# Kernel optimization log

Measured on AMD Instinct MI355X. Metric: run time of the kernel, lower is better.

## Reference

```python
import jax, jax.numpy as jnp
import numpy as np

MODE1 = 12
MODE2 = 12
WIDTH = 64
L = 10
DEPTH = 4
PAD = 9
EPS = 1e-5


def conv1x1(x, w, b):
    # x: (B,Ci,H,W), w: (Co,Ci), b: (Co,)
    return jnp.einsum('oi,bihw->bohw', w, x) + b[None, :, None, None]


def group_norm(x, gamma, beta, groups=2):
    B, C, H, W = x.shape
    xg = x.reshape(B, groups, C // groups, H, W)
    mu = xg.mean(axis=(2, 3, 4), keepdims=True)
    var = xg.var(axis=(2, 3, 4), keepdims=True)
    xn = ((xg - mu) * jax.lax.rsqrt(var + EPS)).reshape(B, C, H, W)
    return xn * gamma[None, :, None, None] + beta[None, :, None, None]


def spectral_conv(x, w1, w2):
    # x: (B,Ci,H,W); w1,w2: (Ci,Co,m1,m2,2) real/imag stacked
    B, Ci, H, W = x.shape
    Co = w1.shape[1]
    x_ft = jnp.fft.rfft2(x)  # (B,Ci,H,W//2+1) complex
    w1c = w1[..., 0] + 1j * w1[..., 1]
    w2c = w2[..., 0] + 1j * w2[..., 1]
    t1 = jnp.einsum('bixy,ioxy->boxy', x_ft[:, :, :MODE1, :MODE2], w1c)
    t2 = jnp.einsum('bixy,ioxy->boxy', x_ft[:, :, -MODE1:, :MODE2], w2c)
    out_ft = jnp.zeros((B, Co, H, W // 2 + 1), dtype=x_ft.dtype)
    out_ft = out_ft.at[:, :, :MODE1, :MODE2].set(t1)
    out_ft = out_ft.at[:, :, -MODE1:, :MODE2].set(t2)
    return jnp.fft.irfft2(out_ft, s=(H, W))


def mlp_block(x, w1, b1, g, bt, w2, b2):
    x = conv1x1(x, w1, b1)
    x = group_norm(x, g, bt)
    x = jax.nn.gelu(x, approximate=False)
    return conv1x1(x, w2, b2)


def get_grid(B, S):
    gx = jnp.linspace(0.0, 1.0, S, dtype=jnp.float32)
    gy = jnp.linspace(0.0, 1.0, S, dtype=jnp.float32)
    gridx = jnp.broadcast_to(gx[None, :, None, None], (B, S, S, 1))
    gridy = jnp.broadcast_to(gy[None, None, :, None], (B, S, S, 1))
    return jnp.concatenate([gridx, gridy], axis=-1)  # (B,S,S,2)


def pos_encoding(grid):
    # grid: (B,S,S,2) -> (B,S,S,4L); cos over all L then sin over all L,
    # within each L the 2 grid channels stay adjacent (matches torch cat order)
    freqs = (jnp.pi * (2.0 ** jnp.arange(L))).astype(jnp.float32)  # (L,)
    phase = grid[..., None, :] * freqs[:, None]  # (B,S,S,L,2)
    B, S1, S2 = grid.shape[:3]
    phase = phase.reshape(B, S1, S2, L * 2)
    return jnp.concatenate([jnp.cos(phase), jnp.sin(phase)], axis=-1)


def setup_inputs() -> dict:
    key = jax.random.key(0)
    ks = jax.random.split(key, 24)
    B, S = 8, 192
    Cin = 3 + 4 * L  # 43
    Wd = WIDTH
    scale = 1.0 / (Wd * Wd)
    d = {}
    d['x'] = jax.random.normal(ks[0], (B, S, S, 1), dtype=jnp.float32)
    d['Wp'] = jax.random.normal(ks[1], (Cin, Wd), dtype=jnp.float32) / np.sqrt(Cin)
    d['bp'] = jnp.zeros((Wd,), dtype=jnp.float32)
    d['sw1'] = scale * jax.random.uniform(ks[2], (DEPTH, Wd, Wd, MODE1, MODE2, 2), dtype=jnp.float32)
    d['sw2'] = scale * jax.random.uniform(ks[3], (DEPTH, Wd, Wd, MODE1, MODE2, 2), dtype=jnp.float32)
    d['m1w'] = jax.random.normal(ks[4], (DEPTH, Wd, Wd), dtype=jnp.float32) / np.sqrt(Wd)
    d['m1b'] = jnp.zeros((DEPTH, Wd), dtype=jnp.float32)
    d['mg'] = jnp.ones((DEPTH, Wd), dtype=jnp.float32)
    d['mbt'] = jnp.zeros((DEPTH, Wd), dtype=jnp.float32)
    d['m2w'] = jax.random.normal(ks[5], (DEPTH, Wd, Wd), dtype=jnp.float32) / np.sqrt(Wd)
    d['m2b'] = jnp.zeros((DEPTH, Wd), dtype=jnp.float32)
    d['ww'] = jax.random.normal(ks[6], (DEPTH, Wd, Wd), dtype=jnp.float32) / np.sqrt(Wd)
    d['wb'] = jnp.zeros((DEPTH, Wd), dtype=jnp.float32)
    d['ng'] = jnp.ones((DEPTH, Wd), dtype=jnp.float32)
    d['nb'] = jnp.zeros((DEPTH, Wd), dtype=jnp.float32)
    Wq = Wd * 4
    d['q1w'] = jax.random.normal(ks[7], (Wq, Wd), dtype=jnp.float32) / np.sqrt(Wd)
    d['q1b'] = jnp.zeros((Wq,), dtype=jnp.float32)
    d['qg'] = jnp.ones((Wq,), dtype=jnp.float32)
    d['qbt'] = jnp.zeros((Wq,), dtype=jnp.float32)
    d['q2w'] = jax.random.normal(ks[8], (1, Wq), dtype=jnp.float32) / np.sqrt(Wq)
    d['q2b'] = jnp.zeros((1,), dtype=jnp.float32)
    return d


def reference(x, Wp, bp, sw1, sw2, m1w, m1b, mg, mbt, m2w, m2b, ww, wb, ng, nb,
              q1w, q1b, qg, qbt, q2w, q2b):
    B, S = x.shape[0], x.shape[1]
    grid = get_grid(B, S)
    pe = pos_encoding(grid)
    h = jnp.concatenate([x, grid, pe], axis=-1)  # (B,S,S,43)
    h = h @ Wp + bp  # lift
    h = h.transpose(0, 3, 1, 2)  # (B,W,S,S)
    h = jnp.pad(h, ((0, 0), (0, 0), (0, PAD), (0, PAD)))
    for i in range(DEPTH):
        x1 = spectral_conv(h, sw1[i], sw2[i])
        x1 = mlp_block(x1, m1w[i], m1b[i], mg[i], mbt[i], m2w[i], m2b[i])
        x2 = conv1x1(h, ww[i], wb[i])
        x2 = group_norm(x2, ng[i], nb[i])
        h = x1 + x2
        if i != DEPTH - 1:
            h = jax.nn.gelu(h, approximate=False)
    h = h[..., :-PAD, :-PAD]
    h = mlp_block(h, q1w, q1b, qg, qbt, q2w, q2b)
    return h.transpose(0, 2, 3, 1)  # (B,S,S,1)
```

## Files before the change

kernel.cpp:

```cpp
#include <hip/hip_runtime.h>
#include <hip/hip_bf16.h>
#include <math.h>


#define NN 201
#define SS 192
#define NPIX 40401
#define QPIX 36864
#define BB 8
#define GNB 80
#define XWPL 1234944
#define PI_F 3.14159265358979323846f

typedef __hip_bfloat16 bf16;
typedef __attribute__((ext_vector_type(8))) short s8v;
typedef __attribute__((ext_vector_type(4))) float f32x4;

__device__ __forceinline__ float gelu_f(float x){
  float x2 = x*x;
  float t  = fmaf(x2, 0.0713548162f, 1.5957691216f);
  float e  = __expf(-x*t);
  return x*__builtin_amdgcn_rcpf(1.0f+e);
}
__device__ __forceinline__ float b2f(bf16 v){ return __bfloat162float(v); }
__device__ __forceinline__ bf16  f2b(float v){ return __float2bfloat16(v); }
__device__ __forceinline__ unsigned short f2bu(float x){
  bf16 h = __float2bfloat16(x);
  unsigned short u; __builtin_memcpy(&u,&h,2); return u;
}
__device__ __forceinline__ float bu2f(unsigned short u){
  unsigned int x = ((unsigned int)u)<<16; float f; __builtin_memcpy(&f,&x,4); return f;
}

__global__ void k_tab(float* __restrict__ tab){
  int t = blockIdx.x*blockDim.x+threadIdx.x;
  if(t>=13*NN) return;
  int k=t/NN, n=t-k*NN;
  int m=(k*n)%NN;
  float ang = (2.0f*PI_F/201.0f)*(float)m;
  tab[2*t]   = cosf(ang);
  tab[2*t+1] = sinf(ang);
}

__global__ void k_tpack(const float* __restrict__ tab, unsigned short* __restrict__ TPK){
  int e = blockIdx.x*256 + threadIdx.x;
  if(e>=6656) return;
  int wt=e>>9, lane=(e>>3)&63, j=e&7;
  int m_=lane&15, g=lane>>4;
  int w = wt*16+m_;
  int k24 = g*8+j;
  float v=0.f;
  if(k24<24 && w<201){
    float2 cs = ((const float2*)tab)[(k24>>1)*NN + w];
    v = (k24&1)? cs.y : cs.x;
  }
  TPK[e]=f2bu(v);
}

__global__ void k_pretab(const float* __restrict__ Wp, const float* __restrict__ bp,
                         float* __restrict__ Ux, float* __restrict__ Uy){
  int i = blockIdx.x;
  int ax = blockIdx.y;
  int c = threadIdx.x;
  float g = (float)i*(1.0f/191.0f);
  float acc;
  if(ax==0) acc = bp[c] + g*Wp[64+c];
  else      acc = g*Wp[128+c];
  int cosBase = (ax==0)? 3 : 4;
  int sinBase = (ax==0)? 23 : 24;
  #pragma unroll
  for(int l=0;l<10;l++){
    float f = PI_F*(float)(1<<l);
    float sv,cv;
    sincosf(g*f,&sv,&cv);
    acc += cv*Wp[(cosBase+2*l)*64+c] + sv*Wp[(sinBase+2*l)*64+c];
  }
  float* U = (ax==0)? Ux : Uy;
  U[i*64+c] = acc;
}

__global__ void k_wpack(const float* __restrict__ m1w, const float* __restrict__ m2w,
                        const float* __restrict__ ww,  const float* __restrict__ q1w,
                        unsigned short* __restrict__ WPK){
  int bx = blockIdx.x, tid = threadIdx.x;
  const float* src;
  if(bx<12){
    int l=bx/3, sel=bx-l*3;
    src = (sel==0)? m1w+(size_t)l*4096 : (sel==1)? m2w+(size_t)l*4096 : ww+(size_t)l*4096;
  } else {
    src = q1w + (size_t)(bx-12)*4096;
  }
  unsigned short* dst = WPK + (size_t)bx*4096;
  #pragma unroll
  for(int t=0;t<16;t++){
    int d = tid*16+t;
    int frag=d>>9, lane=(d>>3)&63, j=d&7;
    int mt=frag>>1, kh=frag&1, m_=lane&15, g=lane>>4;
    dst[d] = f2bu(src[(size_t)(16*mt+m_)*64 + 32*kh + 8*g + j]);
  }
}

__global__ void __launch_bounds__(256) k_wtrans(const float* __restrict__ w1,
        const float* __restrict__ w2, float* __restrict__ WT){
  __shared__ float tile[64][65];
  int io0 = blockIdx.x*64;
  int c0  = blockIdx.y*64;
  int z   = blockIdx.z;
  const float* src = (z==0)? w1 : w2;
  int tid = threadIdx.x;
  #pragma unroll
  for(int it=0;it<16;it++){
    int e = tid + 256*it;
    int r = e>>6, c = e&63;
    if(c0+c<288) tile[r][c] = src[(size_t)(io0+r)*288 + c0 + c];
  }
  __syncthreads();
  #pragma unroll
  for(int it=0;it<16;it++){
    int e = tid + 256*it;
    int rp = e>>6, cp = e&63;
    int col = c0 + rp;
    if(col<288){
      int ky = col/24, rm = col - ky*24;
      int kx = rm>>1, comp = rm&1;
      int m = z*144 + ky*12 + kx;
      WT[(size_t)m*8192 + comp*4096 + io0 + cp] = tile[cp][rp];
    }
  }
}

__global__ void k_encoder(const float* __restrict__ x, const float* __restrict__ Wp,
                          const float* __restrict__ Ux, const float* __restrict__ Uy,
                          bf16* __restrict__ A){
  int tid=threadIdx.x;
  int p = blockIdx.x*256+tid;
  if(p>=NPIX) return;
  int b = blockIdx.y;
  uint4* dst = (uint4*)(A + ((size_t)b*NPIX + p)*64);
  int hh=p/NN, ww=p-hh*NN;
  if(hh>=SS || ww>=SS){
    uint4 z = {0,0,0,0};
    #pragma unroll
    for(int i=0;i<8;i++) dst[i]=z;
    return;
  }
  float xv = x[((size_t)b*SS+hh)*SS+ww];
  const float4* ux = (const float4*)(Ux + hh*64);
  const float4* uy = (const float4*)(Uy + ww*64);
  const float4* w0 = (const float4*)Wp;
  #pragma unroll
  for(int i=0;i<8;i++){
    float4 a0 = ux[2*i],   a1 = ux[2*i+1];
    float4 b0 = uy[2*i],   b1 = uy[2*i+1];
    float4 c0 = w0[2*i],   c1 = w0[2*i+1];
    float v0=xv*c0.x+a0.x+b0.x, v1=xv*c0.y+a0.y+b0.y;
    float v2=xv*c0.z+a0.z+b0.z, v3=xv*c0.w+a0.w+b0.w;
    float v4=xv*c1.x+a1.x+b1.x, v5=xv*c1.y+a1.y+b1.y;
    float v6=xv*c1.z+a1.z+b1.z, v7=xv*c1.w+a1.w+b1.w;
    uint4 v;
    v.x = (unsigned)f2bu(v0) | ((unsigned)f2bu(v1)<<16);
    v.y = (unsigned)f2bu(v2) | ((unsigned)f2bu(v3)<<16);
    v.z = (unsigned)f2bu(v4) | ((unsigned)f2bu(v5)<<16);
    v.w = (unsigned)f2bu(v6) | ((unsigned)f2bu(v7)<<16);
    dst[i]=v;
  }
}

__global__ void __launch_bounds__(256) k_dftw(const bf16* __restrict__ A,
        const float* __restrict__ tab, float* __restrict__ XW){
  __shared__ float2 st[2412];
  int tid=threadIdx.x;
  for(int i=tid;i<2412;i+=256) st[i]=((const float2*)tab)[i];
  __syncthreads();
  int R = blockIdx.x*4 + (tid>>6);
  int l = tid&63;
  const bf16* base = A + ((size_t)R*NN)*64 + l;
  float ar0=0.f;
  float ar[11], ai[11];
  #pragma unroll
  for(int k=0;k<11;k++){ ar[k]=0.f; ai[k]=0.f; }
  for(int w=0;w<NN;w++){
    float a = b2f(base[(size_t)w*64]);
    ar0 += a;
    #pragma unroll
    for(int k=0;k<11;k++){
      float2 cs = st[(k+1)*NN+w];
      ar[k] += a*cs.x;
      ai[k] += a*cs.y;
    }
  }
  float* xre = XW + ((size_t)R*12)*64 + l;
  float* xim = xre + XWPL;
  xre[0]=ar0; xim[0]=0.f;
  #pragma unroll
  for(int k=0;k<11;k++){
    xre[(size_t)(k+1)*64] = ar[k];
    xim[(size_t)(k+1)*64] = -ai[k];
  }
}

__global__ void __launch_bounds__(256) k_dfth(const float* __restrict__ XW,
        const float* __restrict__ tab, float* __restrict__ XF){
  __shared__ float sre[201*32];
  __shared__ float sim[201*32];
  __shared__ float2 tw[13*NN];
  int kx=blockIdx.x, b=blockIdx.y;
  int z=blockIdx.z; int jh=z>>1, ch=z&1;
  int tid=threadIdx.x;
  for(int i=tid;i<13*NN;i+=256) tw[i]=((const float2*)tab)[i];
  for(int i=tid;i<201*32;i+=256){
    int h=i>>5, c=ch*32+(i&31);
    size_t idx=(((size_t)b*NN+h)*12+kx)*64+c;
    sre[i]=XW[idx];
    sim[i]=XW[idx+XWPL];
  }
  __syncthreads();
  for(int o=tid;o<384;o+=256){
    int jj=o>>5, cl=o&31;
    int j=jh*12+jj;
    int k2=(j<12)?j:24-j;
    float sgn=(j<12)?-1.f:1.f;
    float re0=0.f,im0=0.f,re1=0.f,im1=0.f;
    const float* pr=sre+cl;
    const float* pi=sim+cl;
    const float2* tk=tw+k2*NN;
    int h=0;
    for(;h+1<NN;h+=2){
      float a0=pr[h*32], b0=pi[h*32];
      float2 cs0=tk[h];
      float c0=cs0.x, s0=sgn*cs0.y;
      re0 = fmaf(a0,c0, fmaf(-b0,s0, re0));
      im0 = fmaf(a0,s0, fmaf( b0,c0, im0));
      float a1=pr[(h+1)*32], b1=pi[(h+1)*32];
      float2 cs1=tk[h+1];
      float c1=cs1.x, s1=sgn*cs1.y;
      re1 = fmaf(a1,c1, fmaf(-b1,s1, re1));
      im1 = fmaf(a1,s1, fmaf( b1,c1, im1));
    }
    {
      float a0=pr[h*32], b0=pi[h*32];
      float2 cs0=tk[h];
      float c0=cs0.x, s0=sgn*cs0.y;
      re0 = fmaf(a0,c0, fmaf(-b0,s0, re0));
      im0 = fmaf(a0,s0, fmaf( b0,c0, im0));
    }
    int m=j*12+kx;
    int c=ch*32+cl;
    XF[(size_t)m*1024+(b*64+c)*2]  =re0+re1;
    XF[(size_t)m*1024+(b*64+c)*2+1]=im0+im1;
  }
}

__global__ void __launch_bounds__(512) k_modemix(const float* __restrict__ XF,
     const float* __restrict__ WT, float* __restrict__ XO){
  __shared__ float sx[1024];
  __shared__ float swr[4096], swi[4096];
  int m=blockIdx.x;
  int tid=threadIdx.x;
  sx[tid]     = XF[(size_t)m*1024+tid];
  sx[tid+512] = XF[(size_t)m*1024+tid+512];
  const float* wr = WT + (size_t)m*8192;
  const float* wi = wr + 4096;
  for(int io=tid;io<4096;io+=512){
    swr[io]=wr[io];
    swi[io]=wi[io];
  }
  __syncthreads();
  int b=tid>>6, o=tid&63;
  const float* xb = sx + b*128;
  float re0=0.f,re1=0.f,im0=0.f,im1=0.f;
  #pragma unroll 8
  for(int i=0;i<64;i+=2){
    float a=xb[2*i], b2=xb[2*i+1];
    float c=swr[i*64+o], d=swi[i*64+o];
    re0 = fmaf(a,c, fmaf(-b2,d, re0));
    im0 = fmaf(a,d, fmaf( b2,c, im0));
    float a1=xb[2*i+2], b3=xb[2*i+3];
    float c1=swr[(i+1)*64+o], d1=swi[(i+1)*64+o];
    re1 = fmaf(a1,c1, fmaf(-b3,d1, re1));
    im1 = fmaf(a1,d1, fmaf( b3,c1, im1));
  }
  XO[2*((size_t)m*512+tid)]  =re0+re1;
  XO[2*((size_t)m*512+tid)+1]=im0+im1;
}

__global__ void __launch_bounds__(256) k_ispec(const float* __restrict__ XO,
        const float* __restrict__ tab, const unsigned short* __restrict__ TPK,
        bf16* __restrict__ C){
  __shared__ float2 yl[12][64];
  __shared__ float2 cs13[13];
  int R=blockIdx.x;
  int b=R/NN, h=R-b*NN;
  int tid=threadIdx.x;
  if(tid<13) cs13[tid]=((const float2*)tab)[tid*NN+h];
  __syncthreads();
  const float sc = 1.0f/40401.0f;
  #pragma unroll
  for(int it=0;it<3;it++){
    int item = tid + 256*it;
    int kx = item>>6, o = item&63;
    float re0=0.f,im0=0.f,re1=0.f,im1=0.f;
    #pragma unroll
    for(int j=0;j<24;j+=2){
      {
        int k2=(j<12)?j:24-j;
        float sgn=(j<12)?1.0f:-1.0f;
        float2 xo = *(const float2*)(XO + 2*(((size_t)(j*12+kx)*512) + b*64 + o));
        float2 cs = cs13[k2];
        float cc=cs.x, s2=sgn*cs.y;
        re0 = fmaf(xo.x,cc, fmaf(-xo.y,s2, re0));
        im0 = fmaf(xo.x,s2, fmaf( xo.y,cc, im0));
      }
      {
        int j1=j+1;
        int k2=(j1<12)?j1:24-j1;
        float sgn=(j1<12)?1.0f:-1.0f;
        float2 xo = *(const float2*)(XO + 2*(((size_t)(j1*12+kx)*512) + b*64 + o));
        float2 cs = cs13[k2];
        float cc=cs.x, s2=sgn*cs.y;
        re1 = fmaf(xo.x,cc, fmaf(-xo.y,s2, re1));
        im1 = fmaf(xo.x,s2, fmaf( xo.y,cc, im1));
      }
    }
    float fr = (kx==0)? sc : 2.0f*sc;
    float fi = (kx==0)? sc : -2.0f*sc;
    yl[kx][o] = float2{ (re0+re1)*fr, (im0+im1)*fi };
  }
  __syncthreads();
  int wid=tid>>6, l=tid&63, m_=l&15, g=l>>4;
  int o = wid*16 + m_;
  s8v bfr;
  #pragma unroll
  for(int j=0;j<4;j++){
    float2 v = yl[4*g+j][o];
    bfr[2*j]   = (short)f2bu(v.x);
    bfr[2*j+1] = (short)f2bu(v.y);
  }
  bf16* cp = C + (size_t)R*NN*64;
  #pragma unroll
  for(int wt=0; wt<13; wt++){
    s8v af = *(const s8v*)(TPK + (size_t)wt*512 + l*8);
    f32x4 acc = f32x4{0.f,0.f,0.f,0.f};
    acc = __builtin_amdgcn_mfma_f32_16x16x32_bf16(af, bfr, acc, 0,0,0);
    #pragma unroll
    for(int e=0;e<4;e++){
      int w = wt*16 + 4*g + e;
      if(w<NN) cp[(size_t)w*64 + o] = f2b(acc[e]);
    }
  }
}

__global__ void __launch_bounds__(256) k_gramC(const float* __restrict__ XO,
        float* __restrict__ GCp, float* __restrict__ SC){
  __shared__ unsigned short V[64][72];
  int chunk=blockIdx.x, b=blockIdx.y, tid=threadIdx.x;
  const float s1=1.0f/201.0f;
  const float r2=0.70710678118f;
  const float q2=1.41421356237f;
  #pragma unroll
  for(int it=0;it<16;it++){
    int e = tid + it*256;
    int fl=e>>6, ch=e&63;
    int f = chunk*64 + fl;
    int base = b*64+ch;
    float v=0.f;
    if(f<528){
      int comp=f&1, kxm=f>>1;
      int kx0=kxm/24;
      int kx=1+kx0, m=kxm-kx0*24;
      v = q2*XO[2*((size_t)(m*12+kx)*512 + base)+comp];
    } else if(f==528){
      v = XO[2*(size_t)base];
    } else if(f<551){
      int q=f-529; int mm=1+(q>>1);
      const float* p1 = XO + 2*((size_t)(mm*12)*512 + base);
      const float* p2 = XO + 2*((size_t)((24-mm)*12)*512 + base);
      v = ((q&1)==0)? r2*(p1[0]+p2[0]) : r2*(p1[1]-p2[1]);
    } else if(f==551){
      v = r2*XO[2*((size_t)(144)*512 + base)];
    } else if(f==552){
      v = r2*XO[2*((size_t)(144)*512 + base)+1];
    }
    V[ch][fl]=f2bu(v*s1);
  }
  __syncthreads();
  int wid=tid>>6, l=tid&63, m_=l&15, g=l>>4;
  f32x4 acc[4];
  #pragma unroll
  for(int mt=0;mt<4;mt++) acc[mt]=f32x4{0.f,0.f,0.f,0.f};
  #pragma unroll
  for(int kc=0;kc<2;kc++){
    s8v bfr = *(const s8v*)&V[16*wid+m_][kc*32+8*g];
    #pragma unroll
    for(int mt=0;mt<4;mt++){
      s8v afr = *(const s8v*)&V[16*mt+m_][kc*32+8*g];
      acc[mt]=__builtin_amdgcn_mfma_f32_16x16x32_bf16(afr,bfr,acc[mt],0,0,0);
    }
  }
  float* gb = GCp + ((size_t)(b*9+chunk))*4096;
  #pragma unroll
  for(int mt=0;mt<4;mt++){
    #pragma unroll
    for(int e=0;e<4;e++)
      gb[(size_t)(16*mt+4*g+e)*64 + 16*wid + m_] = acc[mt][e];
  }
  if(chunk==0 && tid<64) SC[b*64+tid] = XO[2*(size_t)(b*64+tid)];
}

__global__ void k_gcred(const float* __restrict__ GCp, float* __restrict__ GC){
  int b=blockIdx.y;
  int idx=blockIdx.x*256+threadIdx.x;
  float s=0.f;
  #pragma unroll
  for(int k=0;k<9;k++) s += GCp[((size_t)(b*9+k))*4096 + idx];
  GC[(size_t)b*4096 + idx]=s;
}

__global__ void __launch_bounds__(256) k_gramp(const bf16* __restrict__ X,
        float* __restrict__ Gpart, float* __restrict__ Spart, int HR, int WR){
  int b = blockIdx.y, blk = blockIdx.x;
  int npix = HR*WR;
  int tid=threadIdx.x, wid=tid>>6, l=tid&63;
  int m_=l&15, g=l>>4;
  int slab = blk*4 + wid;
  const bf16* xb = X + (size_t)b*NPIX*64;
  f32x4 acc[4][4];
  #pragma unroll
  for(int mt=0;mt<4;mt++){
    #pragma unroll
    for(int nt=0;nt<4;nt++) acc[mt][nt]=f32x4{0.f,0.f,0.f,0.f};
  }
  float cs[4]={0.f,0.f,0.f,0.f};
  for(int kc=0;kc<16;kc++){
    int pbase = slab*512 + kc*32 + g*8;
    int hh0=0, ww0=0;
    if(WR!=NN){ hh0 = pbase/WR; ww0 = pbase - hh0*WR; }
    const bf16* ptr[8];
    #pragma unroll
    for(int jj=0;jj<8;jj++){
      int p = pbase + jj;
      int gp;
      if(WR==NN) gp = p;
      else {
        int ww2 = ww0 + jj;
        int hh  = hh0;
        if(ww2>=WR){ ww2-=WR; hh++; }
        gp = hh*NN + ww2;
      }
      ptr[jj] = (p<npix) ? (xb + (size_t)gp*64) : (const bf16*)0;
    }
    s8v fr[4];
    #pragma unroll
    for(int t=0;t<4;t++){
      s8v f;
      float s=0.f;
      #pragma unroll
      for(int jj=0;jj<8;jj++){
        unsigned short v=0;
        if(ptr[jj]){ bf16 hv = ptr[jj][16*t+m_]; __builtin_memcpy(&v,&hv,2); }
        f[jj]=(short)v;
        s += bu2f(v);
      }
      fr[t]=f;
      cs[t]+=s;
    }
    #pragma unroll
    for(int nt=0;nt<4;nt++){
      #pragma unroll
      for(int mt=0;mt<4;mt++)
        acc[mt][nt]=__builtin_amdgcn_mfma_f32_16x16x32_bf16(fr[mt],fr[nt],acc[mt][nt],0,0,0);
    }
  }
  float* gp_ = Gpart + ((size_t)(b*GNB + slab))*4096;
  #pragma unroll
  for(int mt=0;mt<4;mt++){
    #pragma unroll
    for(int nt=0;nt<4;nt++){
      #pragma unroll
      for(int e=0;e<4;e++)
        gp_[(size_t)(16*mt + 4*g + e)*64 + 16*nt + m_] = acc[mt][nt][e];
    }
  }
  #pragma unroll
  for(int t=0;t<4;t++){
    float s=cs[t];
    s += __shfl_xor(s,16,64);
    s += __shfl_xor(s,32,64);
    if(g==0) Spart[((size_t)(b*GNB+slab))*64 + 16*t + m_] = s;
  }
}

__global__ void __launch_bounds__(256) k_gramr(const float* __restrict__ Gpart,
        const float* __restrict__ Spart, float* __restrict__ Gfin,
        float* __restrict__ Sfin, int nblk){
  int b = blockIdx.y;
  int idx = blockIdx.x*256 + threadIdx.x;
  float s0=0.f,s1=0.f,s2=0.f,s3=0.f;
  int k=0;
  for(;k+3<nblk;k+=4){
    s0 += Gpart[((size_t)b*GNB + k  )*4096 + idx];
    s1 += Gpart[((size_t)b*GNB + k+1)*4096 + idx];
    s2 += Gpart[((size_t)b*GNB + k+2)*4096 + idx];
    s3 += Gpart[((size_t)b*GNB + k+3)*4096 + idx];
  }
  for(;k<nblk;k++) s0 += Gpart[((size_t)b*GNB + k)*4096 + idx];
  Gfin[(size_t)b*4096 + idx] = (s0+s1)+(s2+s3);
  if(blockIdx.x==0 && threadIdx.x<64){
    float ss=0.f;
    for(int j=0;j<nblk;j++) ss += Spart[((size_t)b*GNB + j)*64 + threadIdx.x];
    Sfin[b*64 + threadIdx.x]=ss;
  }
}

__global__ void __launch_bounds__(256) k_statsA(
        const float* __restrict__ GC, const float* __restrict__ SC,
        const float* __restrict__ Gfin, const float* __restrict__ Sfin,
        const float* __restrict__ m1wl, const float* __restrict__ m1bl,
        const float* __restrict__ wwl,  const float* __restrict__ wbl,
        float* __restrict__ TSTAT, float* __restrict__ USTAT){
  __shared__ float Gs[4096];
  __shared__ float Ss[64];
  __shared__ float rs[256], rq[256];
  int zb=blockIdx.x, t=threadIdx.x;
  const float* GS = (zb<8)? (GC + (size_t)zb*4096) : (Gfin + (size_t)(zb-8)*4096);
  const float* SS_ = (zb<8)? (SC + (size_t)zb*64)   : (Sfin + (size_t)(zb-8)*64);
  #pragma unroll
  for(int e=0;e<16;e++) Gs[t*16+e]=GS[t*16+e];
  if(t<64) Ss[t]=SS_[t];
  __syncthreads();
  const float* W    = (zb<8)? m1wl : wwl;
  const float* bias = (zb<8)? m1bl : wbl;
  float* stat       = (zb<8)? TSTAT : USTAT;
  int b = (zb<8)? zb : zb-8;
  int o = t&63, sl = t>>6;
  float w[64];
  #pragma unroll
  for(int j2=0;j2<64;j2++) w[j2]=bu2f(f2bu(W[(size_t)o*64+j2]));
  const float* Gr = Gs + (size_t)(sl*16)*64;
  float quad=0.f;
  #pragma unroll
  for(int r=0;r<16;r++){
    const float* gr = Gr + r*64;
    float tt=0.f;
    #pragma unroll
    for(int j2=0;j2<64;j2++) tt += gr[j2]*w[j2];
    quad += w[sl*16+r]*tt;
  }
  float dot=0.f;
  #pragma unroll
  for(int j2=0;j2<64;j2++) dot += w[j2]*Ss[j2];
  float bo = bias[o];
  float Nf = (float)NPIX;
  float sm = (sl==0)? (dot + Nf*bo) : 0.f;
  float sq = quad + ((sl==0)? (2.f*bo*dot + Nf*bo*bo) : 0.f);
  rs[t]=sm; rq[t]=sq;
  __syncthreads();
  if(t<64){
    float s2 = rs[t]+rs[t+64]+rs[t+128]+rs[t+192];
    float q2 = rq[t]+rq[t+64]+rq[t+128]+rq[t+192];
    for(int off=16;off>0;off>>=1){
      s2 += __shfl_down(s2,off,32);
      q2 += __shfl_down(q2,off,32);
    }
    if((t&31)==0){
      int g=t>>5;
      float invN = 1.f/(Nf*32.f);
      float mean = s2*invN;
      float var = q2*invN - mean*mean;
      stat[b*4+g*2]   = mean;
      stat[b*4+g*2+1] = rsqrtf(fmaxf(var,0.f)+1e-5f);
    }
  }
}

__global__ void __launch_bounds__(256) k_statsQ(const float* __restrict__ Gfin,
        const float* __restrict__ Sfin,
        const float* __restrict__ W, const float* __restrict__ bias,
        float* __restrict__ stat){
  __shared__ float Gs[4096];
  __shared__ float Ss[64];
  __shared__ float red[8];
  int b=blockIdx.x, t=threadIdx.x;
  #pragma unroll
  for(int e=0;e<16;e++) Gs[t*16+e]=Gfin[(size_t)b*4096 + t*16+e];
  if(t<64) Ss[t]=Sfin[b*64+t];
  __syncthreads();
  float w[64];
  #pragma unroll
  for(int j2=0;j2<64;j2++) w[j2]=bu2f(f2bu(W[(size_t)t*64+j2]));
  float quad=0.f;
  #pragma unroll
  for(int i=0;i<64;i++){
    const float* gr = Gs + i*64;
    float tt=0.f;
    #pragma unroll
    for(int j2=0;j2<64;j2++) tt += gr[j2]*w[j2];
    quad += w[i]*tt;
  }
  float dot=0.f;
  #pragma unroll
  for(int j2=0;j2<64;j2++) dot += w[j2]*Ss[j2];
  float bo=bias[t];
  float Nf=(float)QPIX;
  float sm = dot + Nf*bo;
  float sq = quad + 2.f*bo*dot + Nf*bo*bo;
  for(int off=32;off>0;off>>=1){
    sm += __shfl_down(sm,off,64);
    sq += __shfl_down(sq,off,64);
  }
  int wid=t>>6;
  if((t&63)==0){ red[wid*2]=sm; red[wid*2+1]=sq; }
  __syncthreads();
  if(t<2){
    float smt = red[t*4+0]+red[t*4+2];
    float sqt = red[t*4+1]+red[t*4+3];
    float invN = 1.f/(Nf*128.f);
    float mean = smt*invN;
    float var = sqt*invN - mean*mean;
    stat[b*4+t*2]   = mean;
    stat[b*4+t*2+1] = rsqrtf(fmaxf(var,0.f)+1e-5f);
  }
}

__global__ void __launch_bounds__(256) k_fuse(const bf16* __restrict__ Cb,
    bf16* __restrict__ A,
    const unsigned short* __restrict__ wp1, const float* __restrict__ m1b,
    const float* __restrict__ mg,  const float* __restrict__ mbt,
    const unsigned short* __restrict__ wp2, const float* __restrict__ m2b,
    const unsigned short* __restrict__ wpw, const float* __restrict__ wbk,
    const float* __restrict__ ng,  const float* __restrict__ nb,
    const float* __restrict__ tstat, const float* __restrict__ ustat, int last){
  __shared__ unsigned short vlds[4][64][72];
  int tid=threadIdx.x;
  int wid=tid>>6, l=tid&63;
  int m_=l&15, g=l>>4;
  int b=blockIdx.y;
  int p0=blockIdx.x*256 + wid*64;
  const bf16* cbb = Cb + (size_t)b*NPIX*64;
  const bf16* ab  = A  + (size_t)b*NPIX*64;

  s8v af[4][2];
  f32x4 acc[4][4];

  #pragma unroll
  for(int mt=0;mt<4;mt++){
    #pragma unroll
    for(int kh=0;kh<2;kh++)
      af[mt][kh]=*(const s8v*)(wp1 + (mt*2+kh)*512 + l*8);
    float4 b4 = *(const float4*)(m1b + 16*mt + 4*g);
    #pragma unroll
    for(int nt=0;nt<4;nt++) acc[mt][nt]=f32x4{b4.x,b4.y,b4.z,b4.w};
  }
  #pragma unroll
  for(int nt=0;nt<4;nt++){
    int p = p0 + 16*nt + m_;
    int pc = p<NPIX? p : NPIX-1;
    const s8v* xb = (const s8v*)(cbb + (size_t)pc*64);
    s8v b0 = xb[g], b1 = xb[4+g];
    #pragma unroll
    for(int mt=0;mt<4;mt++){
      acc[mt][nt]=__builtin_amdgcn_mfma_f32_16x16x32_bf16(af[mt][0],b0,acc[mt][nt],0,0,0);
      acc[mt][nt]=__builtin_amdgcn_mfma_f32_16x16x32_bf16(af[mt][1],b1,acc[mt][nt],0,0,0);
    }
  }
  {
    float tm0=tstat[b*4],tr0=tstat[b*4+1],tm1=tstat[b*4+2],tr1=tstat[b*4+3];
    #pragma unroll
    for(int mt=0;mt<4;mt++){
      float4 g4 = *(const float4*)(mg  + 16*mt + 4*g);
      float4 t4 = *(const float4*)(mbt + 16*mt + 4*g);
      float mn = (mt<2)? tm0 : tm1;
      float rs = (mt<2)? tr0 : tr1;
      float ax=rs*g4.x, ay=rs*g4.y, az=rs*g4.z, aw=rs*g4.w;
      float cx=t4.x-mn*ax, cy=t4.y-mn*ay, cz=t4.z-mn*az, cw=t4.w-mn*aw;
      #pragma unroll
      for(int nt=0;nt<4;nt++){
        int pl = 16*nt + m_;
        f32x4 t = acc[mt][nt];
        float v0 = gelu_f(fmaf(t[0],ax,cx));
        float v1 = gelu_f(fmaf(t[1],ay,cy));
        float v2 = gelu_f(fmaf(t[2],az,cz));
        float v3 = gelu_f(fmaf(t[3],aw,cw));
        uint2 pk;
        pk.x = (unsigned)f2bu(v0) | ((unsigned)f2bu(v1)<<16);
        pk.y = (unsigned)f2bu(v2) | ((unsigned)f2bu(v3)<<16);
        *(uint2*)&vlds[wid][pl][16*mt+4*g] = pk;
      }
    }
  }
  __syncthreads();
  #pragma unroll
  for(int mt=0;mt<4;mt++){
    #pragma unroll
    for(int kh=0;kh<2;kh++)
      af[mt][kh]=*(const s8v*)(wpw + (mt*2+kh)*512 + l*8);
    float4 b4 = *(const float4*)(wbk + 16*mt + 4*g);
    #pragma unroll
    for(int nt=0;nt<4;nt++) acc[mt][nt]=f32x4{b4.x,b4.y,b4.z,b4.w};
  }
  #pragma unroll
  for(int nt=0;nt<4;nt++){
    int p = p0 + 16*nt + m_;
    int pc = p<NPIX? p : NPIX-1;
    const s8v* xb = (const s8v*)(ab + (size_t)pc*64);
    s8v b0 = xb[g], b1 = xb[4+g];
    #pragma unroll
    for(int mt=0;mt<4;mt++){
      acc[mt][nt]=__builtin_amdgcn_mfma_f32_16x16x32_bf16(af[mt][0],b0,acc[mt][nt],0,0,0);
      acc[mt][nt]=__builtin_amdgcn_mfma_f32_16x16x32_bf16(af[mt][1],b1,acc[mt][nt],0,0,0);
    }
  }
  {
    float um0=ustat[b*4],ur0=ustat[b*4+1],um1=ustat[b*4+2],ur1=ustat[b*4+3];
    #pragma unroll
    for(int mt=0;mt<4;mt++){
      float4 n4 = *(const float4*)(ng  + 16*mt + 4*g);
      float4 nb4= *(const float4*)(nb  + 16*mt + 4*g);
      float4 m24= *(const float4*)(m2b + 16*mt + 4*g);
      float mn = (mt<2)? um0 : um1;
      float rs = (mt<2)? ur0 : ur1;
      float ax=rs*n4.x, ay=rs*n4.y, az=rs*n4.z, aw=rs*n4.w;
      float cx=m24.x+nb4.x-mn*ax, cy=m24.y+nb4.y-mn*ay;
      float cz=m24.z+nb4.z-mn*az, cw=m24.w+nb4.w-mn*aw;
      #pragma unroll
      for(int nt=0;nt<4;nt++){
        f32x4 u = acc[mt][nt];
        u[0] = fmaf(u[0],ax,cx);
        u[1] = fmaf(u[1],ay,cy);
        u[2] = fmaf(u[2],az,cz);
        u[3] = fmaf(u[3],aw,cw);
        acc[mt][nt]=u;
      }
    }
  }
  #pragma unroll
  for(int mt=0;mt<4;mt++){
    #pragma unroll
    for(int kh=0;kh<2;kh++)
      af[mt][kh]=*(const s8v*)(wp2 + (mt*2+kh)*512 + l*8);
  }
  #pragma unroll
  for(int nt=0;nt<4;nt++){
    int pl = 16*nt + m_;
    const s8v* vp = (const s8v*)&vlds[wid][pl][0];
    s8v b0 = vp[g], b1 = vp[4+g];
    #pragma unroll
    for(int mt=0;mt<4;mt++){
      acc[mt][nt]=__builtin_amdgcn_mfma_f32_16x16x32_bf16(af[mt][0],b0,acc[mt][nt],0,0,0);
      acc[mt][nt]=__builtin_amdgcn_mfma_f32_16x16x32_bf16(af[mt][1],b1,acc[mt][nt],0,0,0);
    }
  }
  #pragma unroll
  for(int nt=0;nt<4;nt++){
    int p = p0 + 16*nt + m_;
    if(p>=NPIX) continue;
    bf16* dp = A + ((size_t)b*NPIX + p)*64;
    #pragma unroll
    for(int mt=0;mt<4;mt++){
      f32x4 h = acc[mt][nt];
      float h0=h[0],h1=h[1],h2=h[2],h3=h[3];
      if(!last){ h0=gelu_f(h0); h1=gelu_f(h1); h2=gelu_f(h2); h3=gelu_f(h3); }
      uint2 pk;
      pk.x = (unsigned)f2bu(h0) | ((unsigned)f2bu(h1)<<16);
      pk.y = (unsigned)f2bu(h2) | ((unsigned)f2bu(h3)<<16);
      *(uint2*)(dp + 16*mt + 4*g) = pk;
    }
  }
}

__global__ void __launch_bounds__(256) k_qout(const bf16* __restrict__ A,
    const unsigned short* __restrict__ qpack, const float* __restrict__ q1b,
    const float* __restrict__ qg, const float* __restrict__ qbt,
    const float* __restrict__ q2w, const float* __restrict__ q2b,
    const float* __restrict__ qstat, float* __restrict__ out){
  __shared__ unsigned short xq[128][72];
  __shared__ float part[4][128];
  int tid=threadIdx.x;
  int wid=tid>>6, l=tid&63;
  int m_=l&15, g=l>>4;
  int b=blockIdx.y;
  int px0=blockIdx.x*128;
  {
    int p = px0 + (tid>>1);
    int half = tid&1;
    int hh=p/SS, ww2=p-hh*SS;
    const uint4* src=(const uint4*)(A + (((size_t)b*NPIX) + (size_t)hh*NN + ww2)*64 + half*32);
    uint4* drow=(uint4*)&xq[tid>>1][half*32];
    #pragma unroll
    for(int i=0;i<4;i++) drow[i]=src[i];
  }
  __syncthreads();
  int oc=wid;
  const unsigned short* wp = qpack + (size_t)oc*4096;
  s8v af[4][2];
  f32x4 bi4[4];
  float4 a4[4], c4[4], w4[4];
  float m0=qstat[b*4],r0=qstat[b*4+1],m1=qstat[b*4+2],r1=qstat[b*4+3];
  float mn=(oc<2)?m0:m1, rs=(oc<2)?r0:r1;
  #pragma unroll
  for(int mt=0;mt<4;mt++){
    #pragma unroll
    for(int kh=0;kh<2;kh++)
      af[mt][kh]=*(const s8v*)(wp + (mt*2+kh)*512 + l*8);
    float4 b4=*(const float4*)(q1b + 64*oc + 16*mt + 4*g);
    bi4[mt]=f32x4{b4.x,b4.y,b4.z,b4.w};
    float4 g4=*(const float4*)(qg  + 64*oc + 16*mt + 4*g);
    float4 t4=*(const float4*)(qbt + 64*oc + 16*mt + 4*g);
    w4[mt]=*(const float4*)(q2w + 64*oc + 16*mt + 4*g);
    a4[mt]=float4{rs*g4.x, rs*g4.y, rs*g4.z, rs*g4.w};
    c4[mt]=float4{t4.x-mn*a4[mt].x, t4.y-mn*a4[mt].y, t4.z-mn*a4[mt].z, t4.w-mn*a4[mt].w};
  }
  #pragma unroll
  for(int nt=0;nt<8;nt++){
    const s8v* vp = (const s8v*)&xq[16*nt+m_][0];
    s8v b0=vp[g], b1=vp[4+g];
    f32x4 acc[4];
    #pragma unroll
    for(int mt=0;mt<4;mt++) acc[mt]=bi4[mt];
    #pragma unroll
    for(int mt=0;mt<4;mt++){
      acc[mt]=__builtin_amdgcn_mfma_f32_16x16x32_bf16(af[mt][0],b0,acc[mt],0,0,0);
      acc[mt]=__builtin_amdgcn_mfma_f32_16x16x32_bf16(af[mt][1],b1,acc[mt],0,0,0);
    }
    float pp=0.f;
    #pragma unroll
    for(int mt=0;mt<4;mt++){
      f32x4 t=acc[mt];
      pp += gelu_f(fmaf(t[0],a4[mt].x,c4[mt].x))*w4[mt].x;
      pp += gelu_f(fmaf(t[1],a4[mt].y,c4[mt].y))*w4[mt].y;
      pp += gelu_f(fmaf(t[2],a4[mt].z,c4[mt].z))*w4[mt].z;
      pp += gelu_f(fmaf(t[3],a4[mt].w,c4[mt].w))*w4[mt].w;
    }
    pp += __shfl_xor(pp,16,64);
    pp += __shfl_xor(pp,32,64);
    if(g==0) part[wid][16*nt+m_]=pp;
  }
  __syncthreads();
  if(tid<128)
    out[(size_t)b*QPIX + px0 + tid] =
        q2b[0] + part[0][tid]+part[1][tid]+part[2][tid]+part[3][tid];
}

extern "C" void kernel_launch(void* const* d_in, const int* in_sizes, int n_in,
                              void* d_out, int out_size, void* d_ws, size_t ws_size,
                              hipStream_t stream){
  const float* x   = (const float*)d_in[0];
  const float* Wp  = (const float*)d_in[1];
  const float* bp  = (const float*)d_in[2];
  const float* sw1 = (const float*)d_in[3];
  const float* sw2 = (const float*)d_in[4];
  const float* m1w = (const float*)d_in[5];
  const float* m1b = (const float*)d_in[6];
  const float* mg  = (const float*)d_in[7];
  const float* mbt = (const float*)d_in[8];
  const float* m2w = (const float*)d_in[9];
  const float* m2b = (const float*)d_in[10];
  const float* ww  = (const float*)d_in[11];
  const float* wb  = (const float*)d_in[12];
  const float* ng  = (const float*)d_in[13];
  const float* nb  = (const float*)d_in[14];
  const float* q1w = (const float*)d_in[15];
  const float* q1b = (const float*)d_in[16];
  const float* qg  = (const float*)d_in[17];
  const float* qbt = (const float*)d_in[18];
  const float* q2w = (const float*)d_in[19];
  const float* q2b = (const float*)d_in[20];
  float* out = (float*)d_out;

  char* w8 = (char*)d_ws;
  const size_t ACT_B = (size_t)64*BB*NPIX*sizeof(bf16);
  bf16*  A    = (bf16*)(w8);
  bf16*  Cb   = (bf16*)(w8 + ACT_B);
  float* SPEC = (float*)(w8 + 2*ACT_B);
  float* XF   = (float*)(w8 + 2*ACT_B + 9879552);
  float* XO   = (float*)(w8 + 2*ACT_B + 9879552 + 1179648);
  float* TB   = (float*)(w8 + 2*ACT_B + 9879552 + 2*1179648);
  char*  g8   = w8 + 2*ACT_B + 9879552 + 2*1179648 + 20992;
  float* TSTAT= (float*)g8;
  float* USTAT= TSTAT + 32;
  float* QSTAT= USTAT + 32;
  float* UxT  = QSTAT + 32;
  float* UyT  = UxT + 12288;
  unsigned short* WPK = (unsigned short*)(UyT + 12288);
  float* GC   = (float*)(WPK + 16*4096);
  float* SC   = GC + 8*4096;
  float* GFIN = SC + 8*64;
  float* SFIN = GFIN + 8*4096;
  unsigned short* TPK = (unsigned short*)(SFIN + 8*64);
  float* GCp  = SPEC;
  float* Gpart = SPEC;
  float* Spart = Gpart + (size_t)8*GNB*4096;
  float* WT = SPEC;
  size_t needed = (size_t)(2*ACT_B) + 9879552 + 2*1179648 + 20992
                + 3*32*4 + 2*12288*4 + 16*4096*2 + 2*(8*4096+8*64)*4 + 13312;
  if(ws_size < needed) return;

  k_tab<<<11,256,0,stream>>>(TB);
  k_tpack<<<26,256,0,stream>>>(TB, TPK);
  k_pretab<<<dim3(192,2),64,0,stream>>>(Wp, bp, UxT, UyT);
  k_wpack<<<16,256,0,stream>>>(m1w, m2w, ww, q1w, WPK);
  k_encoder<<<dim3(158,BB),256,0,stream>>>(x, Wp, UxT, UyT, A);

  for(int l=0;l<4;l++){
    const float* sw1l = sw1 + (size_t)l*1179648;
    const float* sw2l = sw2 + (size_t)l*1179648;
    k_dftw<<<402,256,0,stream>>>(A, TB, SPEC);
    k_dfth<<<dim3(12,BB,4),256,0,stream>>>(SPEC, TB, XF);
    k_wtrans<<<dim3(64,5,2),256,0,stream>>>(sw1l, sw2l, WT);
    k_modemix<<<288,512,0,stream>>>(XF, WT, XO);
    k_ispec<<<1608,256,0,stream>>>(XO, TB, TPK, Cb);
    k_gramC<<<dim3(9,BB),256,0,stream>>>(XO, GCp, SC);
    k_gcred<<<dim3(16,BB),256,0,stream>>>(GCp, GC);
    k_gramp<<<dim3(20,BB),256,0,stream>>>(A, Gpart, Spart, NN, NN);
    k_gramr<<<dim3(16,BB),256,0,stream>>>(Gpart, Spart, GFIN, SFIN, 80);
    k_statsA<<<16,256,0,stream>>>(GC, SC, GFIN, SFIN,
          m1w + (size_t)l*4096, m1b + l*64, ww + (size_t)l*4096, wb + l*64,
          TSTAT, USTAT);
    k_fuse<<<dim3(158,BB),256,0,stream>>>(Cb, A,
          WPK + (size_t)(l*3+0)*4096, m1b + l*64, mg + l*64, mbt + l*64,
          WPK + (size_t)(l*3+1)*4096, m2b + l*64,
          WPK + (size_t)(l*3+2)*4096, wb  + l*64, ng + l*64, nb + l*64,
          TSTAT, USTAT, (l==3)?1:0);
  }

  k_gramp<<<dim3(18,BB),256,0,stream>>>(A, Gpart, Spart, SS, SS);
  k_gramr<<<dim3(16,BB),256,0,stream>>>(Gpart, Spart, GFIN, SFIN, 72);
  k_statsQ<<<BB,256,0,stream>>>(GFIN, SFIN, q1w, q1b, QSTAT);
  k_qout<<<dim3(288,BB),256,0,stream>>>(A, WPK + (size_t)12*4096, q1b,
          qg, qbt, q2w, q2b, QSTAT, out);
}
```

Measured before the change: 981.5 us.

## Compute width-direction truncated DFT with bf16 MFMA instead of scalar FMA

Replaces the scalar per-lane DFT along the width axis in k_dftw with 16x16x32 bf16 MFMA instructions. A new setup kernel prepacks the cos/-sin twiddle table into MFMA A-fragment layout, and the activations are gathered into B fragments in 32-wide chunks with zero padding on the tail. The goal is to cut the FMA-heavy inner loop and its LDS twiddle reads. In exchange the twiddles are rounded to bf16, which loses accuracy, and the strided per-element fragment gathers may limit the benefit.

Result: faster. 885.8 us (-9.7%).

```diff
diff --git a/kernel.cpp b/kernel.cpp
--- a/kernel.cpp
+++ b/kernel.cpp
@@ -55,6 +55,23 @@
     v = (k24&1)? cs.y : cs.x;
   }
   TPK[e]=f2bu(v);
+}
+
+__global__ void k_tpack2(const float* __restrict__ tab, unsigned short* __restrict__ T2PK){
+  int e = blockIdx.x*256 + threadIdx.x;
+  if(e>=7168) return;
+  int idx = e>>9;
+  int mt = idx/7, chunk = idx - mt*7;
+  int lane=(e>>3)&63, j=e&7;
+  int m_=lane&15, g=lane>>4;
+  int kx24 = mt*16 + m_;
+  int w = chunk*32 + g*8 + j;
+  float v=0.f;
+  if(kx24<24 && w<NN){
+    float2 cs = ((const float2*)tab)[(kx24>>1)*NN + w];
+    v = (kx24&1)? -cs.y : cs.x;
+  }
+  T2PK[e]=f2bu(v);
 }
 
 __global__ void k_pretab(const float* __restrict__ Wp, const float* __restrict__ bp,
@@ -167,35 +184,70 @@
 }
 
 __global__ void __launch_bounds__(256) k_dftw(const bf16* __restrict__ A,
-        const float* __restrict__ tab, float* __restrict__ XW){
-  __shared__ float2 st[2412];
-  int tid=threadIdx.x;
-  for(int i=tid;i<2412;i+=256) st[i]=((const float2*)tab)[i];
-  __syncthreads();
-  int R = blockIdx.x*4 + (tid>>6);
-  int l = tid&63;
-  const bf16* base = A + ((size_t)R*NN)*64 + l;
-  float ar0=0.f;
-  float ar[11], ai[11];
-  #pragma unroll
-  for(int k=0;k<11;k++){ ar[k]=0.f; ai[k]=0.f; }
-  for(int w=0;w<NN;w++){
-    float a = b2f(base[(size_t)w*64]);
-    ar0 += a;
-    #pragma unroll
-    for(int k=0;k<11;k++){
-      float2 cs = st[(k+1)*NN+w];
-      ar[k] += a*cs.x;
-      ai[k] += a*cs.y;
-    }
-  }
-  float* xre = XW + ((size_t)R*12)*64 + l;
-  float* xim = xre + XWPL;
-  xre[0]=ar0; xim[0]=0.f;
-  #pragma unroll
-  for(int k=0;k<11;k++){
-    xre[(size_t)(k+1)*64] = ar[k];
-    xim[(size_t)(k+1)*64] = -ai[k];
+        const unsigned short* __restrict__ T2PK, float* __restrict__ XW){
+  int tid=threadIdx.x, wid=tid>>6, l=tid&63;
+  int m_=l&15, g=l>>4;
+  int R = blockIdx.x*4 + wid;
+  const bf16* row = A + (size_t)R*NN*64;
+  f32x4 acc[2][4];
+  #pragma unroll
+  for(int mt=0;mt<2;mt++){
+    #pragma unroll
+    for(int nt=0;nt<4;nt++) acc[mt][nt]=f32x4{0.f,0.f,0.f,0.f};
+  }
+  for(int chunk=0;chunk<7;chunk++){
+    int wbase = chunk*32 + g*8;
+    s8v bf[4];
+    if(chunk<6){
+      #pragma unroll
+      for(int nt=0;nt<4;nt++){
+        s8v f;
+        #pragma unroll
+        for(int j=0;j<8;j++){
+          unsigned short v;
+          bf16 hv = row[(size_t)(wbase+j)*64 + 16*nt + m_];
+          __builtin_memcpy(&v,&hv,2);
+          f[j]=(short)v;
+        }
+        bf[nt]=f;
+      }
+    } else {
+      #pragma unroll
+      for(int nt=0;nt<4;nt++){
+        s8v f;
+        #pragma unroll
+        for(int j=0;j<8;j++){
+          unsigned short v=0;
+          if(wbase+j<NN){
+            bf16 hv = row[(size_t)(wbase+j)*64 + 16*nt + m_];
+            __builtin_memcpy(&v,&hv,2);
+          }
+          f[j]=(short)v;
+        }
+        bf[nt]=f;
+      }
+    }
+    #pragma unroll
+    for(int mt=0;mt<2;mt++){
+      s8v af = *(const s8v*)(T2PK + (size_t)(mt*7+chunk)*512 + l*8);
+      #pragma unroll
+      for(int nt=0;nt<4;nt++)
+        acc[mt][nt]=__builtin_amdgcn_mfma_f32_16x16x32_bf16(af,bf[nt],acc[mt][nt],0,0,0);
+    }
+  }
+  #pragma unroll
+  for(int mt=0;mt<2;mt++){
+    #pragma unroll
+    for(int nt=0;nt<4;nt++){
+      #pragma unroll
+      for(int e=0;e<4;e++){
+        int kx24 = mt*16 + 4*g + e;
+        if(kx24<24){
+          int plane = kx24&1, kx = kx24>>1;
+          XW[(size_t)plane*XWPL + ((size_t)R*12+kx)*64 + 16*nt + m_] = acc[mt][nt][e];
+        }
+      }
+    }
   }
 }
 
@@ -887,16 +939,18 @@
   float* GFIN = SC + 8*64;
   float* SFIN = GFIN + 8*4096;
   unsigned short* TPK = (unsigned short*)(SFIN + 8*64);
+  unsigned short* T2PK = TPK + 6656;
   float* GCp  = SPEC;
   float* Gpart = SPEC;
   float* Spart = Gpart + (size_t)8*GNB*4096;
   float* WT = SPEC;
   size_t needed = (size_t)(2*ACT_B) + 9879552 + 2*1179648 + 20992
-                + 3*32*4 + 2*12288*4 + 16*4096*2 + 2*(8*4096+8*64)*4 + 13312;
+                + 3*32*4 + 2*12288*4 + 16*4096*2 + 2*(8*4096+8*64)*4 + 13312 + 14336;
   if(ws_size < needed) return;
 
   k_tab<<<11,256,0,stream>>>(TB);
   k_tpack<<<26,256,0,stream>>>(TB, TPK);
+  k_tpack2<<<28,256,0,stream>>>(TB, T2PK);
   k_pretab<<<dim3(192,2),64,0,stream>>>(Wp, bp, UxT, UyT);
   k_wpack<<<16,256,0,stream>>>(m1w, m2w, ww, q1w, WPK);
   k_encoder<<<dim3(158,BB),256,0,stream>>>(x, Wp, UxT, UyT, A);
@@ -904,7 +958,7 @@
   for(int l=0;l<4;l++){
     const float* sw1l = sw1 + (size_t)l*1179648;
     const float* sw2l = sw2 + (size_t)l*1179648;
-    k_dftw<<<402,256,0,stream>>>(A, TB, SPEC);
+    k_dftw<<<402,256,0,stream>>>(A, T2PK, SPEC);
     k_dfth<<<dim3(12,BB,4),256,0,stream>>>(SPEC, TB, XF);
     k_wtrans<<<dim3(64,5,2),256,0,stream>>>(sw1l, sw2l, WT);
     k_modemix<<<288,512,0,stream>>>(XF, WT, XO);
```
